# Kernel tuning notes

Hardware: AMD Instinct MI355X
Metric: run time of the kernel (lower is better)

Reference implementation:

```python
import jax, jax.numpy as jnp
import numpy as np

N_NODES = 100000
N_EDGES = 1600000
IN_DIM, HID_DIM, OUT_DIM = 384, 64, 64
DROP_P = 0.5


def setup_inputs() -> dict:
    key = jax.random.key(0)
    ks = jax.random.split(key, 9)
    x = jax.random.normal(ks[0], (N_NODES, IN_DIM), dtype=jnp.float32)
    edge_index = jax.random.randint(ks[1], (2, N_EDGES), 0, N_NODES, dtype=jnp.int64)
    edge_weight = jax.random.uniform(ks[2], (N_EDGES,), dtype=jnp.float32)
    W1 = jax.random.normal(ks[3], (IN_DIM, HID_DIM), dtype=jnp.float32) * (1.0 / np.sqrt(IN_DIM))
    b1 = jnp.zeros((HID_DIM,), dtype=jnp.float32)
    W2 = jax.random.normal(ks[4], (HID_DIM, OUT_DIM), dtype=jnp.float32) * (1.0 / np.sqrt(HID_DIM))
    b2 = jnp.zeros((OUT_DIM,), dtype=jnp.float32)
    drop_mask1 = jax.random.bernoulli(ks[5], 1.0 - DROP_P, (N_NODES, IN_DIM))
    drop_mask2 = jax.random.bernoulli(ks[6], 1.0 - DROP_P, (N_NODES, HID_DIM))
    return {"x": x, "edge_index": edge_index, "edge_weight": edge_weight,
            "W1": W1, "b1": b1, "W2": W2, "b2": b2,
            "drop_mask1": drop_mask1, "drop_mask2": drop_mask2}


def _gcn_conv(h, W, b, src, dst, edge_weight, n_nodes):
    # GCNConv: linear transform first (smaller dim), then normalized sparse aggregation
    h = h @ W                                        # [N, d_out]
    msg = h[src] * edge_weight[:, None]              # gather over edges [E, d_out]
    agg = jax.ops.segment_sum(msg, dst, num_segments=n_nodes)  # scatter-add [N, d_out]
    return agg + b


def reference(x, edge_index, edge_weight, W1, b1, W2, b2, drop_mask1, drop_mask2):
    scale = 1.0 / (1.0 - DROP_P)
    src, dst = edge_index[0], edge_index[1]
    n = x.shape[0]
    h = x * drop_mask1.astype(x.dtype) * scale                  # dropout (training)
    h = jax.nn.relu(_gcn_conv(h, W1, b1, src, dst, edge_weight, n))
    h = h * drop_mask2.astype(h.dtype) * scale                  # dropout (training)
    return _gcn_conv(h, W2, b2, src, dst, edge_weight, n)
```

## Files before the change

kernel.cpp:

```cpp
#include <hip/hip_runtime.h>
#include <hip/hip_bf16.h>
#include <stdint.h>

#define N_NODES 100000
#define N_EDGES 1600000
#define IN_DIM  384
#define HID_DIM 64
#define NPART   8
#define NP      (NPART * N_NODES)
#define SCAN8_NB 782
#define EGRID   2048

typedef __attribute__((ext_vector_type(8))) short short8_t;
typedef __attribute__((ext_vector_type(4))) float f32x4;

__global__ void k_detect(const uint32_t* __restrict__ ei,
                         const uint32_t* __restrict__ m1,
                         int* __restrict__ flags) {
    int l = threadIdx.x;
    uint32_t hi = ei[2 * l + 1];
    int ei64 = __all(hi == 0u);

    uint32_t maxb = 0;
    int bf = 0, f16 = 0, hib = 0;
    for (int i = 0; i < 4; ++i) {
        uint32_t w = m1[l * 4 + i];
        uint32_t b0 = w & 0xffu, b1 = (w >> 8) & 0xffu,
                 b2 = (w >> 16) & 0xffu, b3 = (w >> 24) & 0xffu;
        uint32_t mb = b0 > b1 ? b0 : b1;
        uint32_t mb2 = b2 > b3 ? b2 : b3;
        mb = mb > mb2 ? mb : mb2;
        maxb = maxb > mb ? maxb : mb;
        if ((w & 0xffffu) == 0x3f80u) bf = 1;
        if ((w & 0xffffu) == 0x3c00u) f16 = 1;
        if ((b1 | b2 | b3) != 0u) hib = 1;
    }
    int small  = __all(maxb <= 1u);
    int anybf  = __any(bf);
    int anyf16 = __any(f16);
    int anyhib = __any(hib);
    if (l == 0) {
        flags[0] = ei64;
        int mm;
        if (small)                 mm = anyhib ? 3 : 4;
        else if (anybf || anyf16)  mm = 0;
        else                       mm = 2;
        flags[1] = mm;
    }
}

__device__ __forceinline__ float mask_at(const void* p, int mode, long idx) {
    if (mode == 0) return ((const uint16_t*)p)[idx] ? 2.0f : 0.0f;
    if (mode == 2) return ((const float*)p)[idx] != 0.0f ? 2.0f : 0.0f;
    if (mode == 3) return ((const uint8_t*)p)[idx] ? 2.0f : 0.0f;
    return ((const int*)p)[idx] ? 2.0f : 0.0f;
}

__device__ __forceinline__ void load_edge(const int* p32, int mode64, long e,
                                          int& s, int& d) {
    if (mode64) { s = p32[2 * e]; d = p32[2 * (N_EDGES + e)]; }
    else        { s = p32[e];     d = p32[N_EDGES + e]; }
}

__device__ __forceinline__ ushort f2bf(float f) {
    uint32_t u = __float_as_uint(f);
    return (ushort)((u + 0x7fffu + ((u >> 16) & 1u)) >> 16);
}
__device__ __forceinline__ float bf2f(ushort h) {
    return __uint_as_float(((uint32_t)h) << 16);
}

__global__ __launch_bounds__(256) void k_hist8(const void* __restrict__ ei,
                                               uint32_t* __restrict__ deg8,
                                               const int* __restrict__ flags) {
    const int mode64 = flags[0];
    const int* p32 = (const int*)ei;
    const long pbase = (long)(blockIdx.x & (NPART - 1)) * N_NODES;
    for (long e = (long)blockIdx.x * 256 + threadIdx.x; e < N_EDGES;
         e += (long)EGRID * 256) {
        int s, d; load_edge(p32, mode64, e, s, d);
        atomicAdd(&deg8[pbase + d], 1u);
    }
}

__global__ __launch_bounds__(256) void k_scanA8(const uint32_t* __restrict__ deg,
                                                uint32_t* __restrict__ partials) {
    __shared__ uint32_t sbuf[256];
    long base = (long)blockIdx.x * 1024 + threadIdx.x * 4;
    uint32_t s = 0;
    if (base + 3 < NP) {
        uint4 v = *(const uint4*)&deg[base];
        s = v.x + v.y + v.z + v.w;
    } else {
        for (int j = 0; j < 4; ++j) if (base + j < NP) s += deg[base + j];
    }
    sbuf[threadIdx.x] = s;
    __syncthreads();
    for (int off = 128; off > 0; off >>= 1) {
        if (threadIdx.x < off) sbuf[threadIdx.x] += sbuf[threadIdx.x + off];
        __syncthreads();
    }
    if (threadIdx.x == 0) partials[blockIdx.x] = sbuf[0];
}

__global__ __launch_bounds__(1024) void k_scanB8(const uint32_t* __restrict__ partials,
                                                 uint32_t* __restrict__ poff,
                                                 uint32_t* __restrict__ starts) {
    __shared__ uint32_t sbuf[1024];
    int t = threadIdx.x;
    uint32_t v = t < SCAN8_NB ? partials[t] : 0u;
    sbuf[t] = v;
    __syncthreads();
    for (int off = 1; off < 1024; off <<= 1) {
        uint32_t add = t >= off ? sbuf[t - off] : 0u;
        __syncthreads();
        sbuf[t] += add;
        __syncthreads();
    }
    if (t < SCAN8_NB) poff[t] = sbuf[t] - v;
    if (t == SCAN8_NB - 1) starts[NP] = sbuf[t];
}

__global__ __launch_bounds__(256) void k_scanC8(const uint32_t* __restrict__ deg,
                                                const uint32_t* __restrict__ poff,
                                                uint32_t* __restrict__ starts,
                                                uint32_t* __restrict__ cur) {
    __shared__ uint32_t sbuf[256];
    long base = (long)blockIdx.x * 1024 + threadIdx.x * 4;
    uint32_t v[4] = {0, 0, 0, 0};
    if (base + 3 < NP) {
        uint4 q = *(const uint4*)&deg[base];
        v[0] = q.x; v[1] = q.y; v[2] = q.z; v[3] = q.w;
    } else {
        for (int j = 0; j < 4; ++j) if (base + j < NP) v[j] = deg[base + j];
    }
    uint32_t ts = v[0] + v[1] + v[2] + v[3];
    sbuf[threadIdx.x] = ts;
    __syncthreads();
    for (int off = 1; off < 256; off <<= 1) {
        uint32_t add = threadIdx.x >= off ? sbuf[threadIdx.x - off] : 0u;
        __syncthreads();
        sbuf[threadIdx.x] += add;
        __syncthreads();
    }
    uint32_t run = poff[blockIdx.x] + sbuf[threadIdx.x] - ts;
    for (int j = 0; j < 4; ++j) {
        if (base + j < NP) {
            starts[base + j] = run;
            cur[base + j]    = run;
            run += v[j];
        }
    }
}

__global__ __launch_bounds__(256) void k_reorder8(const void* __restrict__ ei,
                                                  const float* __restrict__ ew,
                                                  uint32_t* __restrict__ cur8,
                                                  int2* __restrict__ sorted,
                                                  const int* __restrict__ flags) {
    const int mode64 = flags[0];
    const int* p32 = (const int*)ei;
    const long pbase = (long)(blockIdx.x & (NPART - 1)) * N_NODES;
    for (long e = (long)blockIdx.x * 256 + threadIdx.x; e < N_EDGES;
         e += (long)EGRID * 256) {
        int s, d; load_edge(p32, mode64, e, s, d);
        float w = ew[e];
        uint32_t pos = atomicAdd(&cur8[pbase + d], 1u);
        sorted[pos] = make_int2(s, __float_as_int(w));
    }
}

__global__ __launch_bounds__(256) void k_packW(const float* __restrict__ W1,
                                               ushort* __restrict__ Wpack) {
    const int ks = blockIdx.x;
    const int t  = threadIdx.x;
    const int nt = t >> 6, l = t & 63;
    ushort hs[8], ls[8];
#pragma unroll
    for (int j = 0; j < 8; ++j) {
        float wv = W1[(ks * 32 + (l >> 4) * 8 + j) * 64 + nt * 16 + (l & 15)];
        ushort h = f2bf(wv);
        hs[j] = h;
        ls[j] = f2bf(wv - bf2f(h));
    }
    *(short8_t*)&Wpack[((8 * ks + nt) * 64 + l) * 8]     = *(short8_t*)hs;
    *(short8_t*)&Wpack[((8 * ks + 4 + nt) * 64 + l) * 8] = *(short8_t*)ls;
}

__global__ __launch_bounds__(256) void k1_mfma(
        const float* __restrict__ x, const void* __restrict__ m1,
        const ushort* __restrict__ Wpack, ushort* __restrict__ Hb,
        const int* __restrict__ flags) {
    const int mmode = flags[1];
    const int t = threadIdx.x;
    const int l = t & 63, w = t >> 6;
    const int node0 = blockIdx.x * 64;
    const long row = node0 + w * 16 + (l & 15);
    const int kq = (l >> 4) * 8;
    const bool valid = row < N_NODES;

    f32x4 acc[4];
#pragma unroll
    for (int i = 0; i < 4; ++i) acc[i] = (f32x4)0.0f;

    for (int ks = 0; ks < 12; ++ks) {
        float xv[8];
        if (valid) {
            long gb = row * IN_DIM + ks * 32 + kq;
            float4 x0 = *(const float4*)(x + gb);
            float4 x1 = *(const float4*)(x + gb + 4);
            xv[0] = x0.x; xv[1] = x0.y; xv[2] = x0.z; xv[3] = x0.w;
            xv[4] = x1.x; xv[5] = x1.y; xv[6] = x1.z; xv[7] = x1.w;
            float mv[8];
            if (mmode == 0) {
                const ushort* mp = (const ushort*)m1 + gb;
                ushort4 a = *(const ushort4*)mp;
                ushort4 b = *(const ushort4*)(mp + 4);
                mv[0] = a.x ? 2.f : 0.f; mv[1] = a.y ? 2.f : 0.f;
                mv[2] = a.z ? 2.f : 0.f; mv[3] = a.w ? 2.f : 0.f;
                mv[4] = b.x ? 2.f : 0.f; mv[5] = b.y ? 2.f : 0.f;
                mv[6] = b.z ? 2.f : 0.f; mv[7] = b.w ? 2.f : 0.f;
            } else if (mmode == 2) {
                const float* mp = (const float*)m1 + gb;
                float4 a = *(const float4*)mp;
                float4 b = *(const float4*)(mp + 4);
                mv[0] = a.x != 0.f ? 2.f : 0.f; mv[1] = a.y != 0.f ? 2.f : 0.f;
                mv[2] = a.z != 0.f ? 2.f : 0.f; mv[3] = a.w != 0.f ? 2.f : 0.f;
                mv[4] = b.x != 0.f ? 2.f : 0.f; mv[5] = b.y != 0.f ? 2.f : 0.f;
                mv[6] = b.z != 0.f ? 2.f : 0.f; mv[7] = b.w != 0.f ? 2.f : 0.f;
            } else if (mmode == 3) {
                uint2 mb = *(const uint2*)((const uint8_t*)m1 + gb);
#pragma unroll
                for (int j = 0; j < 4; ++j) {
                    mv[j]     = ((mb.x >> (8 * j)) & 0xffu) ? 2.f : 0.f;
                    mv[4 + j] = ((mb.y >> (8 * j)) & 0xffu) ? 2.f : 0.f;
                }
            } else {
                const int* mp = (const int*)m1 + gb;
                int4 a = *(const int4*)mp;
                int4 b = *(const int4*)(mp + 4);
                mv[0] = a.x ? 2.f : 0.f; mv[1] = a.y ? 2.f : 0.f;
                mv[2] = a.z ? 2.f : 0.f; mv[3] = a.w ? 2.f : 0.f;
                mv[4] = b.x ? 2.f : 0.f; mv[5] = b.y ? 2.f : 0.f;
                mv[6] = b.z ? 2.f : 0.f; mv[7] = b.w ? 2.f : 0.f;
            }
#pragma unroll
            for (int j = 0; j < 8; ++j) xv[j] *= mv[j];
        } else {
#pragma unroll
            for (int j = 0; j < 8; ++j) xv[j] = 0.0f;
        }
        ushort ap[8];
#pragma unroll
        for (int j = 0; j < 8; ++j) ap[j] = f2bf(xv[j]);
        short8_t ah = *(short8_t*)ap;

#pragma unroll
        for (int nt = 0; nt < 4; ++nt) {
            short8_t bh = *(const short8_t*)&Wpack[((8 * ks + nt) * 64 + l) * 8];
            short8_t bl = *(const short8_t*)&Wpack[((8 * ks + 4 + nt) * 64 + l) * 8];
            acc[nt] = __builtin_amdgcn_mfma_f32_16x16x32_bf16(ah, bh, acc[nt], 0, 0, 0);
            acc[nt] = __builtin_amdgcn_mfma_f32_16x16x32_bf16(ah, bl, acc[nt], 0, 0, 0);
        }
    }
    const int r0 = (l >> 4) * 4;
#pragma unroll
    for (int nt = 0; nt < 4; ++nt) {
#pragma unroll
        for (int r = 0; r < 4; ++r) {
            long node = node0 + w * 16 + r0 + r;
            if (node < N_NODES)
                Hb[node * 64 + nt * 16 + (l & 15)] = f2bf(acc[nt][r]);
        }
    }
}

__device__ __forceinline__ float agg_node(const ushort* __restrict__ Hb,
                                          const int2* __restrict__ sorted,
                                          const uint32_t* __restrict__ starts,
                                          int n, int lane) {
    float acc = 0.0f;
#pragma unroll 1
    for (int p = 0; p < NPART; ++p) {
        uint32_t e  = starts[p * N_NODES + n];
        uint32_t e1 = starts[p * N_NODES + n + 1];
        for (; e + 2 <= e1; e += 2) {
            int2 p0 = sorted[e];
            int2 p1 = sorted[e + 1];
            float v0 = bf2f(Hb[(long)p0.x * 64 + lane]);
            float v1 = bf2f(Hb[(long)p1.x * 64 + lane]);
            acc = fmaf(v0, __int_as_float(p0.y), acc);
            acc = fmaf(v1, __int_as_float(p1.y), acc);
        }
        if (e < e1) {
            int2 p0 = sorted[e];
            acc = fmaf(bf2f(Hb[(long)p0.x * 64 + lane]), __int_as_float(p0.y), acc);
        }
    }
    return acc;
}

__global__ __launch_bounds__(256) void k_aggmlp(
        const ushort* __restrict__ Hb, const int2* __restrict__ sorted,
        const uint32_t* __restrict__ starts, const float* __restrict__ b1,
        const void* __restrict__ m2, const float* __restrict__ W2,
        ushort* __restrict__ H2b, const int* __restrict__ flags) {
    __shared__ float w2s[64 * 64];
    __shared__ float vbuf[4][64];
    const int mmode = flags[1];
    for (int i = threadIdx.x; i < 4096; i += 256) w2s[i] = W2[i];
    __syncthreads();

    const int lane = threadIdx.x & 63;
    const int w = threadIdx.x >> 6;
    const int n = blockIdx.x * 4 + w;
    float acc = agg_node(Hb, sorted, starts, n, lane);
    float u = acc + b1[lane];
    u = u > 0.0f ? u : 0.0f;
    u *= mask_at(m2, mmode, (long)n * 64 + lane);
    vbuf[w][lane] = u;
    float h2 = 0.0f;
#pragma unroll
    for (int j = 0; j < 64; j += 4) {
        float4 v4 = *(const float4*)&vbuf[w][j];
        h2 = fmaf(v4.x, w2s[(j + 0) * 64 + lane], h2);
        h2 = fmaf(v4.y, w2s[(j + 1) * 64 + lane], h2);
        h2 = fmaf(v4.z, w2s[(j + 2) * 64 + lane], h2);
        h2 = fmaf(v4.w, w2s[(j + 3) * 64 + lane], h2);
    }
    H2b[(long)n * 64 + lane] = f2bf(h2);
}

__global__ __launch_bounds__(256) void k_agg(const ushort* __restrict__ Hb,
                                             const int2* __restrict__ sorted,
                                             const uint32_t* __restrict__ starts,
                                             const float* __restrict__ bias,
                                             float* __restrict__ dest) {
    const int lane = threadIdx.x & 63;
    const int n = blockIdx.x * 4 + (threadIdx.x >> 6);
    if (n >= N_NODES) return;
    float acc = bias[lane] + agg_node(Hb, sorted, starts, n, lane);
    dest[(long)n * 64 + lane] = acc;
}

__global__ __launch_bounds__(256) void k_scatter(
        const ushort* __restrict__ Hb, const void* __restrict__ ei,
        const float* __restrict__ ew, float* __restrict__ dest,
        const int* __restrict__ flags) {
    const int mode64 = flags[0];
    const int lane = threadIdx.x & 63;
    const long wid = (long)blockIdx.x * 4 + (threadIdx.x >> 6);
    const long nw = (long)gridDim.x * 4;
    const int* p32 = (const int*)ei;
    for (long e = wid; e < N_EDGES; e += nw) {
        int s, d; load_edge(p32, mode64, e, s, d);
        float w = ew[e];
        float v = bf2f(Hb[(long)s * 64 + lane]) * w;
        atomicAdd(&dest[(long)d * 64 + lane], v);
    }
}

__global__ __launch_bounds__(256) void k3_mlp(
        const float* __restrict__ agg, const float* __restrict__ b1,
        const void* __restrict__ m2, const float* __restrict__ W2,
        ushort* __restrict__ H2b, const int* __restrict__ flags) {
    __shared__ float w2s[64 * 64];
    __shared__ float vbuf[4][64];
    const int mmode = flags[1];
    for (int i = threadIdx.x; i < 4096; i += 256) w2s[i] = W2[i];
    __syncthreads();
    const int lane = threadIdx.x & 63;
    const int w = threadIdx.x >> 6;
    const float bc = b1[lane];
    const long wid = (long)blockIdx.x * 4 + w;
    const long nw = (long)gridDim.x * 4;
    for (long n = wid; n < N_NODES; n += nw) {
        float u = agg[n * 64 + lane] + bc;
        u = u > 0.0f ? u : 0.0f;
        u *= mask_at(m2, mmode, n * 64 + lane);
        vbuf[w][lane] = u;
        float acc = 0.0f;
#pragma unroll
        for (int j = 0; j < 64; j += 4) {
            float4 v4 = *(const float4*)&vbuf[w][j];
            acc = fmaf(v4.x, w2s[(j + 0) * 64 + lane], acc);
            acc = fmaf(v4.y, w2s[(j + 1) * 64 + lane], acc);
            acc = fmaf(v4.z, w2s[(j + 2) * 64 + lane], acc);
            acc = fmaf(v4.w, w2s[(j + 3) * 64 + lane], acc);
        }
        H2b[n * 64 + lane] = f2bf(acc);
    }
}

__global__ void k_init_out(float* __restrict__ out, const float* __restrict__ b2) {
    const long total = (long)N_NODES * 16;
    for (long j = (long)blockIdx.x * 256 + threadIdx.x; j < total;
         j += (long)gridDim.x * 256) {
        ((float4*)out)[j] = ((const float4*)b2)[j & 15];
    }
}

extern "C" void kernel_launch(void* const* d_in, const int* in_sizes, int n_in,
                              void* d_out, int out_size, void* d_ws, size_t ws_size,
                              hipStream_t stream) {
    const float* x  = (const float*)d_in[0];
    const void*  ei = d_in[1];
    const float* ew = (const float*)d_in[2];
    const float* W1 = (const float*)d_in[3];
    const float* b1 = (const float*)d_in[4];
    const float* W2 = (const float*)d_in[5];
    const float* b2 = (const float*)d_in[6];
    const void*  m1 = d_in[7];
    const void*  m2 = d_in[8];
    float* out = (float*)d_out;

    char* ws = (char*)d_ws;
    size_t off = 0;
    auto alloc = [&](size_t bytes) {
        char* p = ws + off;
        off += (bytes + 255) & ~(size_t)255;
        return p;
    };
    int*    flags = (int*)alloc(32);
    ushort* Hb    = (ushort*)alloc((size_t)N_NODES * 64 * 2);
    ushort* H2b   = (ushort*)alloc((size_t)N_NODES * 64 * 2);
    char*   region = alloc((size_t)N_NODES * 64 * 4);
    int2*     sorted = (int2*)region;
    uint32_t* starts = (uint32_t*)(region + (size_t)N_EDGES * 8);
    uint32_t* cur8   = starts + (NP + 64);
    uint32_t* deg8   = cur8 + NP;
    float*    AGG    = (float*)region;
    uint32_t* partials = (uint32_t*)alloc((size_t)SCAN8_NB * 4);
    uint32_t* poff     = (uint32_t*)alloc((size_t)SCAN8_NB * 4);
    ushort*   Wpack    = (ushort*)alloc((size_t)12 * 8 * 64 * 8 * 2);
    size_t need = off;

    hipLaunchKernelGGL(k_detect, dim3(1), dim3(64), 0, stream,
                       (const uint32_t*)ei, (const uint32_t*)m1, flags);
    hipLaunchKernelGGL(k_packW, dim3(12), dim3(256), 0, stream, W1, Wpack);

    if (ws_size >= need) {
        hipMemsetAsync(deg8, 0, (size_t)NP * 4, stream);
        hipLaunchKernelGGL(k_hist8, dim3(EGRID), dim3(256), 0, stream,
                           ei, deg8, flags);
        hipLaunchKernelGGL(k_scanA8, dim3(SCAN8_NB), dim3(256), 0, stream,
                           deg8, partials);
        hipLaunchKernelGGL(k_scanB8, dim3(1), dim3(1024), 0, stream,
                           partials, poff, starts);
        hipLaunchKernelGGL(k_scanC8, dim3(SCAN8_NB), dim3(256), 0, stream,
                           deg8, poff, starts, cur8);
        hipLaunchKernelGGL(k_reorder8, dim3(EGRID), dim3(256), 0, stream,
                           ei, ew, cur8, sorted, flags);
        hipLaunchKernelGGL(k1_mfma, dim3((N_NODES + 63) / 64), dim3(256), 0, stream,
                           x, m1, Wpack, Hb, flags);
        hipLaunchKernelGGL(k_aggmlp, dim3(N_NODES / 4), dim3(256), 0, stream,
                           Hb, sorted, starts, b1, m2, W2, H2b, flags);
        hipLaunchKernelGGL(k_agg, dim3(N_NODES / 4), dim3(256), 0, stream,
                           H2b, sorted, starts, b2, out);
    } else {
        hipMemsetAsync(AGG, 0, (size_t)N_NODES * 64 * 4, stream);
        hipLaunchKernelGGL(k1_mfma, dim3((N_NODES + 63) / 64), dim3(256), 0, stream,
                           x, m1, Wpack, Hb, flags);
        hipLaunchKernelGGL(k_scatter, dim3(4096), dim3(256), 0, stream,
                           Hb, ei, ew, AGG, flags);
        hipLaunchKernelGGL(k3_mlp, dim3(1024), dim3(256), 0, stream,
                           AGG, b1, m2, W2, H2b, flags);
        hipLaunchKernelGGL(k_init_out, dim3(2048), dim3(256), 0, stream, out, b2);
        hipLaunchKernelGGL(k_scatter, dim3(4096), dim3(256), 0, stream,
                           H2b, ei, ew, out, flags);
    }
}
```

Before: 855.9 us.

## Merge 8-partition CSR into a single CSR and use wave-cooperative edge loads

Adds a second pass that sums the per-partition degrees, scans them into a single per-node CSR offset array, and merges the eight partitioned edge segments into one contiguous list per node. The aggregation loops then read each node's edges once: the wave loads up to 64 edge records in one coalesced read, broadcasts them by shuffle, and accumulates into four independent sums. The aim is to drop the per-partition loop overhead and the serial dependent edge loads in the two aggregation kernels. In exchange it adds five extra kernel launches, another full pass over the edge array, and more workspace, and summing into four accumulators changes the floating-point order.

```diff
diff --git a/kernel.cpp b/kernel.cpp
--- a/kernel.cpp
+++ b/kernel.cpp
@@ -9,6 +9,7 @@
 #define NPART   8
 #define NP      (NPART * N_NODES)
 #define SCAN8_NB 782
+#define SCANF_NB 391
 #define EGRID   2048
 
 typedef __attribute__((ext_vector_type(8))) short short8_t;
@@ -151,6 +152,66 @@
             run += v[j];
         }
     }
+}
+
+__global__ __launch_bounds__(256) void k_degsum(const uint32_t* __restrict__ deg8,
+                                                uint32_t* __restrict__ degF) {
+    int n = blockIdx.x * 256 + threadIdx.x;
+    if (n < N_NODES) {
+        uint32_t s = 0;
+#pragma unroll
+        for (int p = 0; p < NPART; ++p) s += deg8[(long)p * N_NODES + n];
+        degF[n] = s;
+    }
+}
+
+__global__ __launch_bounds__(256) void k_scanAF(const uint32_t* __restrict__ deg,
+                                                uint32_t* __restrict__ partials) {
+    __shared__ uint32_t sbuf[256];
+    int idx = blockIdx.x * 256 + threadIdx.x;
+    uint32_t v = idx < N_NODES ? deg[idx] : 0u;
+    sbuf[threadIdx.x] = v;
+    __syncthreads();
+    for (int off = 128; off > 0; off >>= 1) {
+        if (threadIdx.x < off) sbuf[threadIdx.x] += sbuf[threadIdx.x + off];
+        __syncthreads();
+    }
+    if (threadIdx.x == 0) partials[blockIdx.x] = sbuf[0];
+}
+
+__global__ __launch_bounds__(512) void k_scanBF(const uint32_t* __restrict__ partials,
+                                                uint32_t* __restrict__ poff,
+                                                uint32_t* __restrict__ starts) {
+    __shared__ uint32_t sbuf[512];
+    int t = threadIdx.x;
+    uint32_t v = t < SCANF_NB ? partials[t] : 0u;
+    sbuf[t] = v;
+    __syncthreads();
+    for (int off = 1; off < 512; off <<= 1) {
+        uint32_t add = t >= off ? sbuf[t - off] : 0u;
+        __syncthreads();
+        sbuf[t] += add;
+        __syncthreads();
+    }
+    if (t < SCANF_NB) poff[t] = sbuf[t] - v;
+    if (t == SCANF_NB - 1) starts[N_NODES] = sbuf[t];
+}
+
+__global__ __launch_bounds__(256) void k_scanCF(const uint32_t* __restrict__ deg,
+                                                const uint32_t* __restrict__ poff,
+                                                uint32_t* __restrict__ starts) {
+    __shared__ uint32_t sbuf[256];
+    int idx = blockIdx.x * 256 + threadIdx.x;
+    uint32_t v = idx < N_NODES ? deg[idx] : 0u;
+    sbuf[threadIdx.x] = v;
+    __syncthreads();
+    for (int off = 1; off < 256; off <<= 1) {
+        uint32_t add = threadIdx.x >= off ? sbuf[threadIdx.x - off] : 0u;
+        __syncthreads();
+        sbuf[threadIdx.x] += add;
+        __syncthreads();
+    }
+    if (idx < N_NODES) starts[idx] = poff[blockIdx.x] + sbuf[threadIdx.x] - v;
 }
 
 __global__ __launch_bounds__(256) void k_reorder8(const void* __restrict__ ei,
@@ -167,6 +228,47 @@
         float w = ew[e];
         uint32_t pos = atomicAdd(&cur8[pbase + d], 1u);
         sorted[pos] = make_int2(s, __float_as_int(w));
+    }
+}
+
+__global__ __launch_bounds__(256) void k_merge(const int2* __restrict__ tmp,
+                                               const uint32_t* __restrict__ starts8,
+                                               const uint32_t* __restrict__ startsF,
+                                               int2* __restrict__ dst) {
+    const int lane = threadIdx.x & 63;
+    const int n = blockIdx.x * 4 + (threadIdx.x >> 6);
+    uint32_t sv = 0, lv = 0;
+    if (lane < NPART) {
+        sv = starts8[(long)lane * N_NODES + n];
+        lv = starts8[(long)lane * N_NODES + n + 1] - sv;
+    }
+    uint32_t pv = lv;
+#pragma unroll
+    for (int off = 1; off < 8; off <<= 1) {
+        uint32_t t = __shfl_up(pv, off, 64);
+        if (lane >= off) pv += t;
+    }
+    uint32_t ev_ = pv - lv;
+    uint32_t tot = __shfl((int)pv, 7, 64);
+    uint32_t base = startsF[n];
+    uint32_t e1v = __shfl((int)ev_, 1, 64), e2v = __shfl((int)ev_, 2, 64),
+             e3v = __shfl((int)ev_, 3, 64), e4v = __shfl((int)ev_, 4, 64),
+             e5v = __shfl((int)ev_, 5, 64), e6v = __shfl((int)ev_, 6, 64),
+             e7v = __shfl((int)ev_, 7, 64);
+    uint32_t s0v = __shfl((int)sv, 0, 64), s1v = __shfl((int)sv, 1, 64),
+             s2v = __shfl((int)sv, 2, 64), s3v = __shfl((int)sv, 3, 64),
+             s4v = __shfl((int)sv, 4, 64), s5v = __shfl((int)sv, 5, 64),
+             s6v = __shfl((int)sv, 6, 64), s7v = __shfl((int)sv, 7, 64);
+    for (uint32_t i = lane; i < tot; i += 64) {
+        uint32_t eb = 0, sb = s0v;
+        if (i >= e1v) { eb = e1v; sb = s1v; }
+        if (i >= e2v) { eb = e2v; sb = s2v; }
+        if (i >= e3v) { eb = e3v; sb = s3v; }
+        if (i >= e4v) { eb = e4v; sb = s4v; }
+        if (i >= e5v) { eb = e5v; sb = s5v; }
+        if (i >= e6v) { eb = e6v; sb = s6v; }
+        if (i >= e7v) { eb = e7v; sb = s7v; }
+        dst[base + i] = tmp[sb + (i - eb)];
     }
 }
 
@@ -275,29 +377,40 @@
     }
 }
 
-__device__ __forceinline__ float agg_node(const ushort* __restrict__ Hb,
-                                          const int2* __restrict__ sorted,
-                                          const uint32_t* __restrict__ starts,
-                                          int n, int lane) {
-    float acc = 0.0f;
-#pragma unroll 1
-    for (int p = 0; p < NPART; ++p) {
-        uint32_t e  = starts[p * N_NODES + n];
-        uint32_t e1 = starts[p * N_NODES + n + 1];
-        for (; e + 2 <= e1; e += 2) {
-            int2 p0 = sorted[e];
-            int2 p1 = sorted[e + 1];
-            float v0 = bf2f(Hb[(long)p0.x * 64 + lane]);
-            float v1 = bf2f(Hb[(long)p1.x * 64 + lane]);
-            acc = fmaf(v0, __int_as_float(p0.y), acc);
-            acc = fmaf(v1, __int_as_float(p1.y), acc);
-        }
-        if (e < e1) {
-            int2 p0 = sorted[e];
-            acc = fmaf(bf2f(Hb[(long)p0.x * 64 + lane]), __int_as_float(p0.y), acc);
-        }
-    }
-    return acc;
+__device__ __forceinline__ float agg_nodeF(const ushort* __restrict__ Hb,
+                                           const int2* __restrict__ sorted,
+                                           const uint32_t* __restrict__ starts,
+                                           int n, int lane) {
+    uint32_t e = starts[n], e1 = starts[n + 1];
+    float acc0 = 0.f, acc1 = 0.f, acc2 = 0.f, acc3 = 0.f;
+    while (e < e1) {
+        uint32_t rem = e1 - e;
+        uint32_t cnt = rem < 64u ? rem : 64u;
+        uint32_t idx = e + (uint32_t)lane;
+        if (idx >= e1) idx = e1 - 1;
+        int2 my = sorted[idx];
+        uint32_t j = 0;
+        for (; j + 4 <= cnt; j += 4) {
+            int sA = __shfl(my.x, (int)j + 0, 64), wA = __shfl(my.y, (int)j + 0, 64);
+            int sB = __shfl(my.x, (int)j + 1, 64), wB = __shfl(my.y, (int)j + 1, 64);
+            int sC = __shfl(my.x, (int)j + 2, 64), wC = __shfl(my.y, (int)j + 2, 64);
+            int sD = __shfl(my.x, (int)j + 3, 64), wD = __shfl(my.y, (int)j + 3, 64);
+            float vA = bf2f(Hb[(long)sA * 64 + lane]);
+            float vB = bf2f(Hb[(long)sB * 64 + lane]);
+            float vC = bf2f(Hb[(long)sC * 64 + lane]);
+            float vD = bf2f(Hb[(long)sD * 64 + lane]);
+            acc0 = fmaf(vA, __int_as_float(wA), acc0);
+            acc1 = fmaf(vB, __int_as_float(wB), acc1);
+            acc2 = fmaf(vC, __int_as_float(wC), acc2);
+            acc3 = fmaf(vD, __int_as_float(wD), acc3);
+        }
+        for (; j < cnt; ++j) {
+            int sA = __shfl(my.x, (int)j, 64), wA = __shfl(my.y, (int)j, 64);
+            acc0 = fmaf(bf2f(Hb[(long)sA * 64 + lane]), __int_as_float(wA), acc0);
+        }
+        e += cnt;
+    }
+    return (acc0 + acc1) + (acc2 + acc3);
 }
 
 __global__ __launch_bounds__(256) void k_aggmlp(
@@ -314,7 +427,7 @@
     const int lane = threadIdx.x & 63;
     const int w = threadIdx.x >> 6;
     const int n = blockIdx.x * 4 + w;
-    float acc = agg_node(Hb, sorted, starts, n, lane);
+    float acc = agg_nodeF(Hb, sorted, starts, n, lane);
     float u = acc + b1[lane];
     u = u > 0.0f ? u : 0.0f;
     u *= mask_at(m2, mmode, (long)n * 64 + lane);
@@ -339,7 +452,7 @@
     const int lane = threadIdx.x & 63;
     const int n = blockIdx.x * 4 + (threadIdx.x >> 6);
     if (n >= N_NODES) return;
-    float acc = bias[lane] + agg_node(Hb, sorted, starts, n, lane);
+    float acc = bias[lane] + agg_nodeF(Hb, sorted, starts, n, lane);
     dest[(long)n * 64 + lane] = acc;
 }
 
@@ -424,15 +537,19 @@
     int*    flags = (int*)alloc(32);
     ushort* Hb    = (ushort*)alloc((size_t)N_NODES * 64 * 2);
     ushort* H2b   = (ushort*)alloc((size_t)N_NODES * 64 * 2);
-    char*   region = alloc((size_t)N_NODES * 64 * 4);
-    int2*     sorted = (int2*)region;
-    uint32_t* starts = (uint32_t*)(region + (size_t)N_EDGES * 8);
-    uint32_t* cur8   = starts + (NP + 64);
-    uint32_t* deg8   = cur8 + NP;
-    float*    AGG    = (float*)region;
-    uint32_t* partials = (uint32_t*)alloc((size_t)SCAN8_NB * 4);
-    uint32_t* poff     = (uint32_t*)alloc((size_t)SCAN8_NB * 4);
-    ushort*   Wpack    = (ushort*)alloc((size_t)12 * 8 * 64 * 8 * 2);
+    int2*   sorted8 = (int2*)alloc((size_t)N_EDGES * 8);
+    int2*   sortedF = (int2*)alloc((size_t)N_EDGES * 8);
+    float*  AGG   = (float*)sorted8;
+    uint32_t* starts8 = (uint32_t*)alloc((size_t)(NP + 64) * 4);
+    uint32_t* cur8    = (uint32_t*)alloc((size_t)NP * 4);
+    uint32_t* deg8    = (uint32_t*)alloc((size_t)NP * 4);
+    uint32_t* degF    = (uint32_t*)alloc((size_t)N_NODES * 4);
+    uint32_t* startsF = (uint32_t*)alloc((size_t)(N_NODES + 64) * 4);
+    uint32_t* part8   = (uint32_t*)alloc((size_t)SCAN8_NB * 4);
+    uint32_t* poff8   = (uint32_t*)alloc((size_t)SCAN8_NB * 4);
+    uint32_t* partF   = (uint32_t*)alloc((size_t)SCANF_NB * 4);
+    uint32_t* poffF   = (uint32_t*)alloc((size_t)SCANF_NB * 4);
+    ushort*   Wpack   = (ushort*)alloc((size_t)12 * 8 * 64 * 8 * 2);
     size_t need = off;
 
     hipLaunchKernelGGL(k_detect, dim3(1), dim3(64), 0, stream,
@@ -444,19 +561,29 @@
         hipLaunchKernelGGL(k_hist8, dim3(EGRID), dim3(256), 0, stream,
                            ei, deg8, flags);
         hipLaunchKernelGGL(k_scanA8, dim3(SCAN8_NB), dim3(256), 0, stream,
-                           deg8, partials);
+                           deg8, part8);
         hipLaunchKernelGGL(k_scanB8, dim3(1), dim3(1024), 0, stream,
-                           partials, poff, starts);
+                           part8, poff8, starts8);
         hipLaunchKernelGGL(k_scanC8, dim3(SCAN8_NB), dim3(256), 0, stream,
-                           deg8, poff, starts, cur8);
+                           deg8, poff8, starts8, cur8);
         hipLaunchKernelGGL(k_reorder8, dim3(EGRID), dim3(256), 0, stream,
-                           ei, ew, cur8, sorted, flags);
+                           ei, ew, cur8, sorted8, flags);
+        hipLaunchKernelGGL(k_degsum, dim3(SCANF_NB), dim3(256), 0, stream,
+                           deg8, degF);
+        hipLaunchKernelGGL(k_scanAF, dim3(SCANF_NB), dim3(256), 0, stream,
+                           degF, partF);
+        hipLaunchKernelGGL(k_scanBF, dim3(1), dim3(512), 0, stream,
+                           partF, poffF, startsF);
+        hipLaunchKernelGGL(k_scanCF, dim3(SCANF_NB), dim3(256), 0, stream,
+                           degF, poffF, startsF);
+        hipLaunchKernelGGL(k_merge, dim3(N_NODES / 4), dim3(256), 0, stream,
+                           sorted8, starts8, startsF, sortedF);
         hipLaunchKernelGGL(k1_mfma, dim3((N_NODES + 63) / 64), dim3(256), 0, stream,
                            x, m1, Wpack, Hb, flags);
         hipLaunchKernelGGL(k_aggmlp, dim3(N_NODES / 4), dim3(256), 0, stream,
-                           Hb, sorted, starts, b1, m2, W2, H2b, flags);
+                           Hb, sortedF, startsF, b1, m2, W2, H2b, flags);
         hipLaunchKernelGGL(k_agg, dim3(N_NODES / 4), dim3(256), 0, stream,
-                           H2b, sorted, starts, b2, out);
+                           H2b, sortedF, startsF, b2, out);
     } else {
         hipMemsetAsync(AGG, 0, (size_t)N_NODES * 64 * 4, stream);
         hipLaunchKernelGGL(k1_mfma, dim3((N_NODES + 63) / 64), dim3(256), 0, stream,
```

Result: faster. 718.9 us (-16.0%).
